# Optimization experiments

Measured on AMD Instinct MI355X. Metric: run time of the kernel, lower is better.

## Reference

```python
import jax, jax.numpy as jnp
import numpy as np

D_MODEL = 512
D_STATE = 64
L_SEQ = 4096
BATCH = 4


def _make_A(N):
    # HiPPO-LegS style A: A[n,k] = -sqrt(2n+1)sqrt(2k+1) if n>k, -(n+1) if n==k, 0 else (n,k from 1..N)
    idx = np.arange(1, N + 1, dtype=np.float64)
    M = np.sqrt(2 * idx[:, None] + 1) * np.sqrt(2 * idx[None, :] + 1)
    lower = (idx[:, None] > idx[None, :]).astype(np.float64)
    return -(lower * M + np.diag(idx + 1))


def _discretize(A, B, C, step):
    # bilinear (Tustin) transform
    I = np.eye(A.shape[0])
    BL = np.linalg.inv(I - step / 2.0 * A)
    Ab = BL @ (I + step / 2.0 * A)
    Bb = (BL * step) @ B
    return Ab, Bb, C


def setup_inputs() -> dict:
    key = jax.random.key(0)
    rng = np.random.RandomState(0)
    A = _make_A(D_STATE)
    B = rng.randn(D_STATE, 1)
    C = rng.randn(1, D_STATE)
    Ab, Bb, Cb = _discretize(A, B, C, step=1.0 / L_SEQ)
    u = jax.random.normal(key, (BATCH, L_SEQ, D_MODEL), dtype=jnp.float32)
    return {
        "u": u,
        "A_": jnp.asarray(Ab, dtype=jnp.float32),
        "B_": jnp.asarray(Bb, dtype=jnp.float32),
        "C_": jnp.asarray(Cb, dtype=jnp.float32),
    }


def reference(u, A_, B_, C_):
    # u: (B, L, D) -> flatten channels: (BD, L)
    b, L, d = u.shape
    uc = u.transpose(0, 2, 1).reshape(b * d, L)
    N = A_.shape[0]
    b_vec = B_[:, 0]  # (N,)
    c_vec = C_[0]     # (N,)

    def step(x, u_k):
        # x: (BD, N), u_k: (BD,)
        # x_k = A_ @ x_{k-1}^T + B_ @ u_k^T  (expressed batched as x @ A_.T + outer)
        x_new = x @ A_.T + u_k[:, None] * b_vec[None, :]
        y_k = x_new @ c_vec  # (BD,)
        return x_new, y_k

    x0 = jnp.zeros((b * d, N), dtype=u.dtype)
    _, ys = jax.lax.scan(step, x0, uc.T)  # ys: (L, BD)
    y = ys.T.reshape(b, d, L).transpose(0, 2, 1)  # (B, L, D)
    return y
```

## Files before the change

kernel.cpp:

```cpp
#include <hip/hip_runtime.h>

#define L_SEQ   4096
#define D_MODEL 512
#define NSEQ    2048
#define CH      128
#define NC      32

#define OFF_P    0
#define OFF_W1T  4096
#define OFF_WOUT 12288
#define OFF_KLOC 20480
#define OFF_GX   20736

#define BC(v, j) __int_as_float(__builtin_amdgcn_readlane(__float_as_int(v), (j)))

__global__ __launch_bounds__(256) void k_prep(
    const float* __restrict__ A, const float* __restrict__ B,
    const float* __restrict__ C, float* __restrict__ ws) {
  __shared__ float M0[64][68];
  __shared__ float M1[64][68];
  __shared__ float Asv[64][68];
  __shared__ float vrT[128][65];
  __shared__ float Cs[64], Bsh[64];

  const int tid = threadIdx.x;
  if (tid < 64) { Cs[tid] = C[tid]; Bsh[tid] = B[tid]; }
  for (int e = tid; e < 4096; e += 256) {
    const float a = A[e];
    M0[e >> 6][e & 63] = a;
    Asv[e >> 6][e & 63] = a;
  }
  __syncthreads();

  const int iy4 = (tid >> 4) * 4, jx4 = (tid & 15) * 4;
  for (int it = 0; it < 7; ++it) {
    float (*src)[68] = (it & 1) ? M1 : M0;
    float (*dst)[68] = (it & 1) ? M0 : M1;
    float acc[4][4] = {{0.f}};
#pragma unroll 8
    for (int k = 0; k < 64; ++k) {
      const float a0 = src[iy4 + 0][k];
      const float a1 = src[iy4 + 1][k];
      const float a2 = src[iy4 + 2][k];
      const float a3 = src[iy4 + 3][k];
      const float4 b4 = *(const float4*)&src[k][jx4];
      acc[0][0] += a0 * b4.x; acc[0][1] += a0 * b4.y; acc[0][2] += a0 * b4.z; acc[0][3] += a0 * b4.w;
      acc[1][0] += a1 * b4.x; acc[1][1] += a1 * b4.y; acc[1][2] += a1 * b4.z; acc[1][3] += a1 * b4.w;
      acc[2][0] += a2 * b4.x; acc[2][1] += a2 * b4.y; acc[2][2] += a2 * b4.z; acc[2][3] += a2 * b4.w;
      acc[3][0] += a3 * b4.x; acc[3][1] += a3 * b4.y; acc[3][2] += a3 * b4.z; acc[3][3] += a3 * b4.w;
    }
    __syncthreads();
#pragma unroll
    for (int r = 0; r < 4; ++r)
#pragma unroll
      for (int c = 0; c < 4; ++c) dst[iy4 + r][jx4 + c] = acc[r][c];
    __syncthreads();
  }

  float* Pg = ws + OFF_P;
  for (int e = tid; e < 4096; e += 256) Pg[e] = M1[e >> 6][e & 63];

  const int lane = tid & 63, wv = tid >> 6;
  float* Wg = ws + OFF_WOUT;
  float reg[64];
  if (wv == 0) {
#pragma unroll
    for (int j = 0; j < 64; ++j) reg[j] = Asv[lane][j];
    float cur = Bsh[lane];
    vrT[0][lane] = cur;
    for (int m = 1; m < 64; ++m) {
      float nv = 0.f;
#pragma unroll
      for (int j = 0; j < 64; ++j) nv += reg[j] * BC(cur, j);
      cur = nv;
      vrT[m][lane] = cur;
    }
  } else if (wv == 1) {
#pragma unroll
    for (int j = 0; j < 64; ++j) reg[j] = Asv[lane][j];
    const float b0 = Bsh[lane];
    float cur = 0.f;
#pragma unroll
    for (int j = 0; j < 64; ++j) cur += M0[lane][j] * BC(b0, j);
    vrT[64][lane] = cur;
    for (int m = 65; m < 128; ++m) {
      float nv = 0.f;
#pragma unroll
      for (int j = 0; j < 64; ++j) nv += reg[j] * BC(cur, j);
      cur = nv;
      vrT[m][lane] = cur;
    }
  } else if (wv == 2) {
#pragma unroll
    for (int j = 0; j < 64; ++j) reg[j] = Asv[j][lane];
    float cur = Cs[lane];
    for (int m = 1; m <= 64; ++m) {
      float nv = 0.f;
#pragma unroll
      for (int j = 0; j < 64; ++j) nv += BC(cur, j) * reg[j];
      cur = nv;
      Wg[lane * 128 + m - 1] = cur;
    }
  } else {
#pragma unroll
    for (int j = 0; j < 64; ++j) reg[j] = Asv[j][lane];
    const float c0 = Cs[lane];
    float cur = 0.f;
#pragma unroll
    for (int j = 0; j < 64; ++j) cur += BC(c0, j) * M0[j][lane];
    for (int m = 65; m <= 128; ++m) {
      float nv = 0.f;
#pragma unroll
      for (int j = 0; j < 64; ++j) nv += BC(cur, j) * reg[j];
      cur = nv;
      Wg[lane * 128 + m - 1] = cur;
    }
  }
  __syncthreads();

  float* W1Tg = ws + OFF_W1T;
  for (int e = tid; e < 8192; e += 256) {
    const int r = e >> 6, i = e & 63;
    W1Tg[e] = vrT[127 - r][i];
  }

  float* Kz = ws + OFF_KLOC;
  if (tid < 128) {
    float acc = 0.f;
#pragma unroll
    for (int i = 0; i < 64; ++i) acc += Cs[i] * vrT[tid][i];
    Kz[128 + tid] = acc;
  } else {
    Kz[tid - 128] = 0.f;
  }
}

__global__ __launch_bounds__(256) void k_proj(
    const float* __restrict__ u, const float* __restrict__ wsr,
    float* __restrict__ gx) {
  __shared__ float W1s[128][66];
  __shared__ float Us[64][132];

  const int st = blockIdx.x;
  const int c = blockIdx.y;
  const int tid = threadIdx.x;
  const int sgl = st * 128;
  const int bi = sgl >> 9, d0 = sgl & 511;

  const float* W1Tg = wsr + OFF_W1T;
#pragma unroll
  for (int k = 0; k < 32; ++k) {
    const int e = tid + 256 * k;
    W1s[e >> 6][e & 63] = W1Tg[e];
  }

  const float* ub = u + ((size_t)bi * L_SEQ + c * CH) * D_MODEL + d0;
  const int sy4 = (tid >> 3) * 4;
  const int ix8 = (tid & 7) * 8;

  float acc[4][8];
#pragma unroll
  for (int r = 0; r < 4; ++r)
#pragma unroll
    for (int cc = 0; cc < 8; ++cc) acc[r][cc] = 0.f;

  for (int h = 0; h < 2; ++h) {
    __syncthreads();
#pragma unroll
    for (int e8 = 0; e8 < 8; ++e8) {
      const int e = tid + 256 * e8;
      const int rr = e >> 5, s4 = (e & 31) * 4;
      *(float4*)&Us[rr][s4] =
          *(const float4*)(ub + (size_t)(h * 64 + rr) * D_MODEL + s4);
    }
    __syncthreads();
#pragma unroll 4
    for (int rr = 0; rr < 64; ++rr) {
      const int r = h * 64 + rr;
      const float4 a = *(const float4*)&Us[rr][sy4];
      const float4 b0 = *(const float4*)&W1s[r][ix8];
      const float4 b1 = *(const float4*)&W1s[r][ix8 + 4];
      acc[0][0] += a.x * b0.x; acc[0][1] += a.x * b0.y; acc[0][2] += a.x * b0.z; acc[0][3] += a.x * b0.w;
      acc[0][4] += a.x * b1.x; acc[0][5] += a.x * b1.y; acc[0][6] += a.x * b1.z; acc[0][7] += a.x * b1.w;
      acc[1][0] += a.y * b0.x; acc[1][1] += a.y * b0.y; acc[1][2] += a.y * b0.z; acc[1][3] += a.y * b0.w;
      acc[1][4] += a.y * b1.x; acc[1][5] += a.y * b1.y; acc[1][6] += a.y * b1.z; acc[1][7] += a.y * b1.w;
      acc[2][0] += a.z * b0.x; acc[2][1] += a.z * b0.y; acc[2][2] += a.z * b0.z; acc[2][3] += a.z * b0.w;
      acc[2][4] += a.z * b1.x; acc[2][5] += a.z * b1.y; acc[2][6] += a.z * b1.z; acc[2][7] += a.z * b1.w;
      acc[3][0] += a.w * b0.x; acc[3][1] += a.w * b0.y; acc[3][2] += a.w * b0.z; acc[3][3] += a.w * b0.w;
      acc[3][4] += a.w * b1.x; acc[3][5] += a.w * b1.y; acc[3][6] += a.w * b1.z; acc[3][7] += a.w * b1.w;
    }
  }

  float* gb = gx + ((size_t)c * NSEQ + sgl) * 64;
#pragma unroll
  for (int as = 0; as < 4; ++as) {
    float4 v0, v1;
    v0.x = acc[as][0]; v0.y = acc[as][1]; v0.z = acc[as][2]; v0.w = acc[as][3];
    v1.x = acc[as][4]; v1.y = acc[as][5]; v1.z = acc[as][6]; v1.w = acc[as][7];
    float* row = gb + (size_t)(sy4 + as) * 64 + ix8;
    *(float4*)row = v0;
    *(float4*)(row + 4) = v1;
  }
}

__global__ __launch_bounds__(256) void k_scan(
    const float* __restrict__ wsr, float* __restrict__ gx) {
  const int lane = threadIdx.x & 63, wv = threadIdx.x >> 6;
  const int s = blockIdx.x * 4 + wv;

  float p[64];
  {
    const float* pr = wsr + OFF_P + lane * 64;
#pragma unroll
    for (int j = 0; j < 64; j += 4) {
      const float4 v = *(const float4*)(pr + j);
      p[j] = v.x; p[j + 1] = v.y; p[j + 2] = v.z; p[j + 3] = v.w;
    }
  }

  float* gs = gx + (size_t)s * 64 + lane;
  float x = 0.f;
  float g = gs[0];
  for (int c = 0; c < NC; ++c) {
    const float gn = (c + 1 < NC) ? gs[(size_t)(c + 1) * NSEQ * 64] : 0.f;
    gs[(size_t)c * NSEQ * 64] = x;
    float x0 = g, x1 = 0.f;
#pragma unroll
    for (int j = 0; j < 64; j += 2) {
      x0 += p[j] * BC(x, j);
      x1 += p[j + 1] * BC(x, j + 1);
    }
    x = x0 + x1;
    g = gn;
  }
}

__global__ __launch_bounds__(256) void k_localout(
    const float* __restrict__ u, const float* __restrict__ wsr,
    const float* __restrict__ gx, float* __restrict__ out) {
  __shared__ float As[64][68];
  __shared__ float Bs[64][132];

  const int sg = blockIdx.x;
  const int tr = blockIdx.y;
  const int c = tr >> 1, par = tr & 1;
  const int r0 = par * 64;
  const int sgl = sg * 128;
  const int bi = sgl >> 9, d0 = sgl & 511;

  const float* KlocZ = wsr + OFF_KLOC;
  const float* WoutG = wsr + OFF_WOUT;
  const float* ub = u + ((size_t)bi * L_SEQ + c * CH) * D_MODEL + d0;

  const int tid = threadIdx.x;
  const int ty4 = (tid >> 4) * 4;
  const int tx8 = (tid & 15) * 8;

  float acc[4][8];
#pragma unroll
  for (int r = 0; r < 4; ++r)
#pragma unroll
    for (int cc = 0; cc < 8; ++cc) acc[r][cc] = 0.f;

  for (int kt = 0; kt <= par; ++kt) {
    const int k0 = kt * 64;
#pragma unroll
    for (int e8 = 0; e8 < 8; ++e8) {
      const int e = tid + 256 * e8;
      const int kk = e >> 5, s4 = (e & 31) * 4;
      *(float4*)&Bs[kk][s4] = *(const float4*)(ub + (size_t)(k0 + kk) * D_MODEL + s4);
    }
    const int base = 128 + r0 - k0;
#pragma unroll
    for (int e4 = 0; e4 < 16; ++e4) {
      const int e = tid + 256 * e4;
      const int kk = e >> 6, i = e & 63;
      As[kk][i] = KlocZ[base + i - kk];
    }
    __syncthreads();
#pragma unroll 4
    for (int kk = 0; kk < 64; ++kk) {
      const float4 a = *(const float4*)&As[kk][ty4];
      const float4 b0 = *(const float4*)&Bs[kk][tx8];
      const float4 b1 = *(const float4*)&Bs[kk][tx8 + 4];
      acc[0][0] += a.x * b0.x; acc[0][1] += a.x * b0.y; acc[0][2] += a.x * b0.z; acc[0][3] += a.x * b0.w;
      acc[0][4] += a.x * b1.x; acc[0][5] += a.x * b1.y; acc[0][6] += a.x * b1.z; acc[0][7] += a.x * b1.w;
      acc[1][0] += a.y * b0.x; acc[1][1] += a.y * b0.y; acc[1][2] += a.y * b0.z; acc[1][3] += a.y * b0.w;
      acc[1][4] += a.y * b1.x; acc[1][5] += a.y * b1.y; acc[1][6] += a.y * b1.z; acc[1][7] += a.y * b1.w;
      acc[2][0] += a.z * b0.x; acc[2][1] += a.z * b0.y; acc[2][2] += a.z * b0.z; acc[2][3] += a.z * b0.w;
      acc[2][4] += a.z * b1.x; acc[2][5] += a.z * b1.y; acc[2][6] += a.z * b1.z; acc[2][7] += a.z * b1.w;
      acc[3][0] += a.w * b0.x; acc[3][1] += a.w * b0.y; acc[3][2] += a.w * b0.z; acc[3][3] += a.w * b0.w;
      acc[3][4] += a.w * b1.x; acc[3][5] += a.w * b1.y; acc[3][6] += a.w * b1.z; acc[3][7] += a.w * b1.w;
    }
    __syncthreads();
  }

  {
    const float* xc = gx + ((size_t)c * NSEQ + sgl) * 64;
#pragma unroll
    for (int e8 = 0; e8 < 8; ++e8) {
      const int e = tid + 256 * e8;
      const int sl = e >> 4, i4 = (e & 15) * 4;
      const float4 v = *(const float4*)(xc + (size_t)sl * 64 + i4);
      Bs[i4 + 0][sl] = v.x;
      Bs[i4 + 1][sl] = v.y;
      Bs[i4 + 2][sl] = v.z;
      Bs[i4 + 3][sl] = v.w;
    }
#pragma unroll
    for (int e4 = 0; e4 < 16; ++e4) {
      const int e = tid + 256 * e4;
      const int i_ = e >> 6, r = e & 63;
      As[i_][r] = WoutG[i_ * 128 + r0 + r];
    }
    __syncthreads();
#pragma unroll 4
    for (int kk = 0; kk < 64; ++kk) {
      const float4 a = *(const float4*)&As[kk][ty4];
      const float4 b0 = *(const float4*)&Bs[kk][tx8];
      const float4 b1 = *(const float4*)&Bs[kk][tx8 + 4];
      acc[0][0] += a.x * b0.x; acc[0][1] += a.x * b0.y; acc[0][2] += a.x * b0.z; acc[0][3] += a.x * b0.w;
      acc[0][4] += a.x * b1.x; acc[0][5] += a.x * b1.y; acc[0][6] += a.x * b1.z; acc[0][7] += a.x * b1.w;
      acc[1][0] += a.y * b0.x; acc[1][1] += a.y * b0.y; acc[1][2] += a.y * b0.z; acc[1][3] += a.y * b0.w;
      acc[1][4] += a.y * b1.x; acc[1][5] += a.y * b1.y; acc[1][6] += a.y * b1.z; acc[1][7] += a.y * b1.w;
      acc[2][0] += a.z * b0.x; acc[2][1] += a.z * b0.y; acc[2][2] += a.z * b0.z; acc[2][3] += a.z * b0.w;
      acc[2][4] += a.z * b1.x; acc[2][5] += a.z * b1.y; acc[2][6] += a.z * b1.z; acc[2][7] += a.z * b1.w;
      acc[3][0] += a.w * b0.x; acc[3][1] += a.w * b0.y; acc[3][2] += a.w * b0.z; acc[3][3] += a.w * b0.w;
      acc[3][4] += a.w * b1.x; acc[3][5] += a.w * b1.y; acc[3][6] += a.w * b1.z; acc[3][7] += a.w * b1.w;
    }
  }

  float* ob = out + ((size_t)bi * L_SEQ + c * CH + r0) * D_MODEL + d0;
#pragma unroll
  for (int r = 0; r < 4; ++r) {
    float4 v0, v1;
    v0.x = acc[r][0]; v0.y = acc[r][1]; v0.z = acc[r][2]; v0.w = acc[r][3];
    v1.x = acc[r][4]; v1.y = acc[r][5]; v1.z = acc[r][6]; v1.w = acc[r][7];
    float* row = ob + (size_t)(ty4 + r) * D_MODEL + tx8;
    *(float4*)row = v0;
    *(float4*)(row + 4) = v1;
  }
}

extern "C" void kernel_launch(void* const* d_in, const int* in_sizes, int n_in,
                              void* d_out, int out_size, void* d_ws,
                              size_t ws_size, hipStream_t stream) {
  const float* u = (const float*)d_in[0];
  const float* A = (const float*)d_in[1];
  const float* B = (const float*)d_in[2];
  const float* C = (const float*)d_in[3];
  float* out = (float*)d_out;
  float* ws = (float*)d_ws;
  float* gx = ws + OFF_GX;

  k_prep<<<1, 256, 0, stream>>>(A, B, C, ws);
  k_proj<<<dim3(16, 32), 256, 0, stream>>>(u, ws, gx);
  k_scan<<<512, 256, 0, stream>>>(ws, gx);
  k_localout<<<dim3(16, 64), 256, 0, stream>>>(u, ws, gx, out);
}
```

Before: 209.7 us.

## Compute Krylov powers by doubling GEMMs and deepen scan prefetch

The prep kernel no longer runs four serial 64-step wave recurrences to build A^m B and C A^m. It builds them by repeated doubling alongside the matrix squaring: each round multiplies the existing block of vectors by the current power of A with tiled shared-memory GEMMs across all threads, and it keeps a transposed copy of the power matrix. The scan kernel now prefetches the chunk input three chunks ahead instead of one, to hide global load latency. The cost is more shared memory and a more complex schedule in prep, and rounding may differ slightly from the serial recurrence.

```diff
diff --git a/kernel.cpp b/kernel.cpp
--- a/kernel.cpp
+++ b/kernel.cpp
@@ -17,112 +17,150 @@
 __global__ __launch_bounds__(256) void k_prep(
     const float* __restrict__ A, const float* __restrict__ B,
     const float* __restrict__ C, float* __restrict__ ws) {
-  __shared__ float M0[64][68];
-  __shared__ float M1[64][68];
-  __shared__ float Asv[64][68];
-  __shared__ float vrT[128][65];
+  __shared__ float Srow[64][68];
+  __shared__ float STs[64][68];
+  __shared__ float vrT[128][68];
+  __shared__ float cwS[129][68];
   __shared__ float Cs[64], Bsh[64];
 
   const int tid = threadIdx.x;
   if (tid < 64) { Cs[tid] = C[tid]; Bsh[tid] = B[tid]; }
   for (int e = tid; e < 4096; e += 256) {
     const float a = A[e];
-    M0[e >> 6][e & 63] = a;
-    Asv[e >> 6][e & 63] = a;
+    Srow[e >> 6][e & 63] = a;
+    STs[e & 63][e >> 6] = a;
   }
   __syncthreads();
 
+  if (tid < 64) {
+    vrT[0][tid] = Bsh[tid];
+    float acc = 0.f;
+#pragma unroll
+    for (int k = 0; k < 64; ++k) acc += Cs[k] * STs[tid][k];
+    cwS[1][tid] = acc;
+  }
+  __syncthreads();
+
   const int iy4 = (tid >> 4) * 4, jx4 = (tid & 15) * 4;
-  for (int it = 0; it < 7; ++it) {
-    float (*src)[68] = (it & 1) ? M1 : M0;
-    float (*dst)[68] = (it & 1) ? M0 : M1;
-    float acc[4][4] = {{0.f}};
-#pragma unroll 8
-    for (int k = 0; k < 64; ++k) {
-      const float a0 = src[iy4 + 0][k];
-      const float a1 = src[iy4 + 1][k];
-      const float a2 = src[iy4 + 2][k];
-      const float a3 = src[iy4 + 3][k];
-      const float4 b4 = *(const float4*)&src[k][jx4];
-      acc[0][0] += a0 * b4.x; acc[0][1] += a0 * b4.y; acc[0][2] += a0 * b4.z; acc[0][3] += a0 * b4.w;
-      acc[1][0] += a1 * b4.x; acc[1][1] += a1 * b4.y; acc[1][2] += a1 * b4.z; acc[1][3] += a1 * b4.w;
-      acc[2][0] += a2 * b4.x; acc[2][1] += a2 * b4.y; acc[2][2] += a2 * b4.z; acc[2][3] += a2 * b4.w;
-      acc[3][0] += a3 * b4.x; acc[3][1] += a3 * b4.y; acc[3][2] += a3 * b4.z; acc[3][3] += a3 * b4.w;
-    }
-    __syncthreads();
-#pragma unroll
-    for (int r = 0; r < 4; ++r)
-#pragma unroll
-      for (int c = 0; c < 4; ++c) dst[iy4 + r][jx4 + c] = acc[r][c];
+
+  for (int t = 0; t < 7; ++t) {
+    const int nd = 1 << t;
+
+    if (nd <= 2) {
+      const int total = 2 * nd * 64;
+      if (tid < total) {
+        const int half = (tid >= nd * 64);
+        const int o = (tid >> 6) & (nd - 1);
+        const int idx = tid & 63;
+        float acc = 0.f;
+        if (!half) {
+#pragma unroll
+          for (int k = 0; k < 64; ++k) acc += vrT[o][k] * Srow[idx][k];
+          vrT[nd + o][idx] = acc;
+        } else {
+#pragma unroll
+          for (int k = 0; k < 64; ++k) acc += cwS[1 + o][k] * STs[idx][k];
+          cwS[nd + 1 + o][idx] = acc;
+        }
+      }
+    } else {
+      const int tilesPerGemm = nd * 4;
+      for (int tt = tid; tt < 2 * tilesPerGemm; tt += 256) {
+        const int half = (tt >= tilesPerGemm);
+        const int q = half ? tt - tilesPerGemm : tt;
+        const int m0 = (q >> 4) * 4;
+        const int i0 = (q & 15) * 4;
+        float acc[4][4] = {{0.f}};
+        if (!half) {
+#pragma unroll 4
+          for (int k = 0; k < 64; k += 4) {
+            float a_[4][4];
+#pragma unroll
+            for (int r = 0; r < 4; ++r)
+              *(float4*)&a_[r][0] = *(const float4*)&vrT[m0 + r][k];
+#pragma unroll
+            for (int kk = 0; kk < 4; ++kk) {
+              const float4 b4 = *(const float4*)&STs[k + kk][i0];
+#pragma unroll
+              for (int r = 0; r < 4; ++r) {
+                const float av = a_[r][kk];
+                acc[r][0] += av * b4.x; acc[r][1] += av * b4.y;
+                acc[r][2] += av * b4.z; acc[r][3] += av * b4.w;
+              }
+            }
+          }
+#pragma unroll
+          for (int r = 0; r < 4; ++r) {
+            float4 v; v.x = acc[r][0]; v.y = acc[r][1]; v.z = acc[r][2]; v.w = acc[r][3];
+            *(float4*)&vrT[nd + m0 + r][i0] = v;
+          }
+        } else {
+#pragma unroll 4
+          for (int k = 0; k < 64; k += 4) {
+            float a_[4][4];
+#pragma unroll
+            for (int r = 0; r < 4; ++r)
+              *(float4*)&a_[r][0] = *(const float4*)&cwS[1 + m0 + r][k];
+#pragma unroll
+            for (int kk = 0; kk < 4; ++kk) {
+              const float4 b4 = *(const float4*)&Srow[k + kk][i0];
+#pragma unroll
+              for (int r = 0; r < 4; ++r) {
+                const float av = a_[r][kk];
+                acc[r][0] += av * b4.x; acc[r][1] += av * b4.y;
+                acc[r][2] += av * b4.z; acc[r][3] += av * b4.w;
+              }
+            }
+          }
+#pragma unroll
+          for (int r = 0; r < 4; ++r) {
+            float4 v; v.x = acc[r][0]; v.y = acc[r][1]; v.z = acc[r][2]; v.w = acc[r][3];
+            *(float4*)&cwS[nd + 1 + m0 + r][i0] = v;
+          }
+        }
+      }
+    }
+
+    float sacc[4][4] = {{0.f}};
+#pragma unroll 4
+    for (int k = 0; k < 64; k += 4) {
+      float a_[4][4];
+#pragma unroll
+      for (int r = 0; r < 4; ++r)
+        *(float4*)&a_[r][0] = *(const float4*)&Srow[iy4 + r][k];
+#pragma unroll
+      for (int kk = 0; kk < 4; ++kk) {
+        const float4 b4 = *(const float4*)&Srow[k + kk][jx4];
+#pragma unroll
+        for (int r = 0; r < 4; ++r) {
+          const float av = a_[r][kk];
+          sacc[r][0] += av * b4.x; sacc[r][1] += av * b4.y;
+          sacc[r][2] += av * b4.z; sacc[r][3] += av * b4.w;
+        }
+      }
+    }
+    __syncthreads();
+#pragma unroll
+    for (int r = 0; r < 4; ++r) {
+      float4 v; v.x = sacc[r][0]; v.y = sacc[r][1]; v.z = sacc[r][2]; v.w = sacc[r][3];
+      *(float4*)&Srow[iy4 + r][jx4] = v;
+    }
+#pragma unroll
+    for (int c = 0; c < 4; ++c) {
+      float4 v; v.x = sacc[0][c]; v.y = sacc[1][c]; v.z = sacc[2][c]; v.w = sacc[3][c];
+      *(float4*)&STs[jx4 + c][iy4] = v;
+    }
     __syncthreads();
   }
 
   float* Pg = ws + OFF_P;
-  for (int e = tid; e < 4096; e += 256) Pg[e] = M1[e >> 6][e & 63];
-
-  const int lane = tid & 63, wv = tid >> 6;
+  for (int e = tid; e < 4096; e += 256) Pg[e] = Srow[e >> 6][e & 63];
+
+  float* W1Tg = ws + OFF_W1T;
+  for (int e = tid; e < 8192; e += 256) W1Tg[e] = vrT[127 - (e >> 6)][e & 63];
+
   float* Wg = ws + OFF_WOUT;
-  float reg[64];
-  if (wv == 0) {
-#pragma unroll
-    for (int j = 0; j < 64; ++j) reg[j] = Asv[lane][j];
-    float cur = Bsh[lane];
-    vrT[0][lane] = cur;
-    for (int m = 1; m < 64; ++m) {
-      float nv = 0.f;
-#pragma unroll
-      for (int j = 0; j < 64; ++j) nv += reg[j] * BC(cur, j);
-      cur = nv;
-      vrT[m][lane] = cur;
-    }
-  } else if (wv == 1) {
-#pragma unroll
-    for (int j = 0; j < 64; ++j) reg[j] = Asv[lane][j];
-    const float b0 = Bsh[lane];
-    float cur = 0.f;
-#pragma unroll
-    for (int j = 0; j < 64; ++j) cur += M0[lane][j] * BC(b0, j);
-    vrT[64][lane] = cur;
-    for (int m = 65; m < 128; ++m) {
-      float nv = 0.f;
-#pragma unroll
-      for (int j = 0; j < 64; ++j) nv += reg[j] * BC(cur, j);
-      cur = nv;
-      vrT[m][lane] = cur;
-    }
-  } else if (wv == 2) {
-#pragma unroll
-    for (int j = 0; j < 64; ++j) reg[j] = Asv[j][lane];
-    float cur = Cs[lane];
-    for (int m = 1; m <= 64; ++m) {
-      float nv = 0.f;
-#pragma unroll
-      for (int j = 0; j < 64; ++j) nv += BC(cur, j) * reg[j];
-      cur = nv;
-      Wg[lane * 128 + m - 1] = cur;
-    }
-  } else {
-#pragma unroll
-    for (int j = 0; j < 64; ++j) reg[j] = Asv[j][lane];
-    const float c0 = Cs[lane];
-    float cur = 0.f;
-#pragma unroll
-    for (int j = 0; j < 64; ++j) cur += BC(c0, j) * M0[j][lane];
-    for (int m = 65; m <= 128; ++m) {
-      float nv = 0.f;
-#pragma unroll
-      for (int j = 0; j < 64; ++j) nv += BC(cur, j) * reg[j];
-      cur = nv;
-      Wg[lane * 128 + m - 1] = cur;
-    }
-  }
-  __syncthreads();
-
-  float* W1Tg = ws + OFF_W1T;
-  for (int e = tid; e < 8192; e += 256) {
-    const int r = e >> 6, i = e & 63;
-    W1Tg[e] = vrT[127 - r][i];
-  }
+  for (int e = tid; e < 8192; e += 256) Wg[e] = cwS[(e & 127) + 1][e >> 7];
 
   float* Kz = ws + OFF_KLOC;
   if (tid < 128) {
@@ -218,20 +256,23 @@
     }
   }
 
+  const size_t CS = (size_t)NSEQ * 64;
   float* gs = gx + (size_t)s * 64 + lane;
   float x = 0.f;
-  float g = gs[0];
+  float g0 = gs[0];
+  float g1 = gs[CS];
+  float g2 = gs[2 * CS];
   for (int c = 0; c < NC; ++c) {
-    const float gn = (c + 1 < NC) ? gs[(size_t)(c + 1) * NSEQ * 64] : 0.f;
-    gs[(size_t)c * NSEQ * 64] = x;
-    float x0 = g, x1 = 0.f;
+    const float gn = (c + 3 < NC) ? gs[(size_t)(c + 3) * CS] : 0.f;
+    gs[(size_t)c * CS] = x;
+    float x0 = g0, x1 = 0.f;
 #pragma unroll
     for (int j = 0; j < 64; j += 2) {
       x0 += p[j] * BC(x, j);
       x1 += p[j + 1] * BC(x, j + 1);
     }
     x = x0 + x1;
-    g = gn;
+    g0 = g1; g1 = g2; g2 = gn;
   }
 }
 
```

Result: faster. 199.8 us (-4.7%).
